# Optimization experiments

Hardware: AMD Instinct MI355X
Metric: run time of the kernel (lower is better)

The kernel has to match this reference:

```python
import jax, jax.numpy as jnp
import numpy as np

N_BATCH = 1024   # batch size (P=256 identities x K=4 instances)
M_PARTS = 8      # local stripes per image
D_FEAT = 128     # local feature dim
K_PER_ID = 4
MARGIN = 0.3
EPS = 1e-12


def setup_inputs() -> dict:
    key = jax.random.key(0)
    inputs = jax.random.normal(key, (N_BATCH, M_PARTS, D_FEAT), dtype=jnp.float32)
    labels = jnp.arange(N_BATCH, dtype=jnp.int64) // K_PER_ID  # equal samples per class
    return {"inputs": inputs, "labels": labels}


def _shortest_dist(dmat):
    """DTW-style monotone shortest path over the (m, n) grid.
    dmat: [m, n, N, N] -> returns [N, N].
    """
    m = dmat.shape[0]
    # first row: only moves to the right -> cumulative sum over j
    row = jnp.cumsum(dmat[0], axis=0)  # [n, N, N]
    inf = jnp.full(dmat.shape[2:], jnp.inf, dtype=dmat.dtype)

    def step(carry, inp):
        d_ij, up = inp                       # each [N, N]
        val = jnp.minimum(carry, up) + d_ij  # carry=inf at j=0 -> picks `up`
        return val, val

    for i in range(1, m):  # m is a small structural constant (stripes)
        _, row = jax.lax.scan(step, inf, (dmat[i], row))
    return row[-1]  # dist[m-1][n-1], shape [N, N]


def _local_dist(x):
    """x: [N, m, d] (already L2-normalized) -> pairwise aligned dist [N, N]."""
    N, m, d = x.shape
    xf = x.reshape(N * m, d)
    sq = jnp.sum(xf * xf, axis=1)
    dist = sq[:, None] + sq[None, :] - 2.0 * (xf @ xf.T)   # [Nm, Nm]
    dist = jnp.sqrt(jnp.clip(dist, EPS, None))
    dist = jnp.tanh(dist * 0.5)  # (e^d - 1) / (e^d + 1)
    dist = dist.reshape(N, m, N, m).transpose(1, 3, 0, 2)   # [m, n, N, N]
    return _shortest_dist(dist)


def reference(inputs, labels):
    # normalize local features to unit length
    x = inputs / (jnp.linalg.norm(inputs, axis=-1, keepdims=True) + EPS)
    dist_mat = _local_dist(x)  # [N, N]

    # hard example mining
    is_pos = labels[:, None] == labels[None, :]
    dist_ap = jnp.max(jnp.where(is_pos, dist_mat, -jnp.inf), axis=1)
    dist_an = jnp.min(jnp.where(is_pos, jnp.inf, dist_mat), axis=1)

    # MarginRankingLoss(margin)(dist_an, dist_ap, y=1)
    loss = jnp.mean(jnp.maximum(dist_ap - dist_an + MARGIN, 0.0))
    return loss
```

## Files before the change

### kernel.cpp

```cpp
#include <hip/hip_runtime.h>
#include <hip/hip_bf16.h>
#include <math.h>

#define NB 1024
#define MP 8
#define DF 128
#define NV (NB*MP)
#define EPSR 1e-12f
#define MARGIN_ 0.3f

#define GC0  0.4999965f
#define GC1 -0.0416276f
#define GC2  0.0040808f
#define GC3 -0.00035138f
#define GC4  0.00001765f

typedef __bf16 bf16x8 __attribute__((ext_vector_type(8)));
typedef float  f32x4  __attribute__((ext_vector_type(4)));

__global__ __launch_bounds__(256) void norm_kernel(const float* __restrict__ x,
                                                   unsigned short* __restrict__ xnb,
                                                   unsigned* __restrict__ ap_max,
                                                   unsigned* __restrict__ an_min) {
    if (blockIdx.x == 0) {
        for (int i = threadIdx.x; i < NB; i += 256) {
            ap_max[i] = 0u;
            an_min[i] = 0x7F800000u;
        }
    }
    const int wave = threadIdx.x >> 6;
    const int lane = threadIdx.x & 63;
    const int v = blockIdx.x * 4 + wave;
    const float e0 = x[v * DF + lane];
    const float e1 = x[v * DF + 64 + lane];
    float s = e0 * e0 + e1 * e1;
    #pragma unroll
    for (int off = 32; off > 0; off >>= 1) s += __shfl_xor(s, off);
    const float inv = 1.0f / (sqrtf(s) + EPSR);
    const __hip_bfloat16 b0 = __float2bfloat16(e0 * inv);
    const __hip_bfloat16 b1 = __float2bfloat16(e1 * inv);
    xnb[v * DF + lane]      = *(const unsigned short*)&b0;
    xnb[v * DF + 64 + lane] = *(const unsigned short*)&b1;
}

__global__ __launch_bounds__(256) void dist_kernel(const unsigned short* __restrict__ xnb,
                                                   const int* __restrict__ labels,
                                                   unsigned* __restrict__ ap_max,
                                                   unsigned* __restrict__ an_min) {
    __shared__ alignas(16) unsigned char smem[65536];
    unsigned short* As = (unsigned short*)smem;
    unsigned short* Bs = (unsigned short*)(smem + 32768);
    float* E = (float*)smem;

    const int idx = (int)blockIdx.x;
    float fsq = sqrtf(8.0f * (float)idx + 1.0f);
    int by = (int)((fsq - 1.0f) * 0.5f);
    while ((by + 1) * (by + 2) / 2 <= idx) ++by;
    while (by * (by + 1) / 2 > idx) --by;
    const int bx = idx - by * (by + 1) / 2;

    const int t    = threadIdx.x;
    const int wave = t >> 6;
    const int lane = t & 63;
    const int wr   = wave >> 1;
    const int wc   = wave & 1;
    const int aBase = bx * 16;
    const int bBase = by * 16;

    #pragma unroll
    for (int i = 0; i < 8; ++i) {
        const int ldi = t + i * 256;
        const int row = ldi >> 4;
        const int ch  = ldi & 15;
        const int p   = ch ^ (row & 15);
        const uint4 va = *(const uint4*)&xnb[(aBase * MP + row) * DF + ch * 8];
        const uint4 vb = *(const uint4*)&xnb[(bBase * MP + row) * DF + ch * 8];
        *(uint4*)&As[row * DF + p * 8] = va;
        *(uint4*)&Bs[row * DF + p * 8] = vb;
    }
    __syncthreads();

    f32x4 acc[4][4];
    #pragma unroll
    for (int tr = 0; tr < 4; ++tr)
        #pragma unroll
        for (int tc = 0; tc < 4; ++tc) acc[tr][tc] = (f32x4){0.f, 0.f, 0.f, 0.f};

    const int fr = lane & 15;
    const int fq = lane >> 4;
    #pragma unroll
    for (int ks = 0; ks < 4; ++ks) {
        bf16x8 af[4], bfr[4];
        const int ch = ks * 4 + fq;
        #pragma unroll
        for (int tr = 0; tr < 4; ++tr) {
            const int va = wr * 64 + tr * 16 + fr;
            af[tr] = *(const bf16x8*)&As[va * DF + (ch ^ fr) * 8];
        }
        #pragma unroll
        for (int tc = 0; tc < 4; ++tc) {
            const int vb = wc * 64 + tc * 16 + fr;
            bfr[tc] = *(const bf16x8*)&Bs[vb * DF + (ch ^ fr) * 8];
        }
        #pragma unroll
        for (int tr = 0; tr < 4; ++tr)
            #pragma unroll
            for (int tc = 0; tc < 4; ++tc)
                acc[tr][tc] = __builtin_amdgcn_mfma_f32_16x16x32_bf16(
                    af[tr], bfr[tc], acc[tr][tc], 0, 0, 0);
    }
    __syncthreads();

    #pragma unroll
    for (int tr = 0; tr < 4; ++tr) {
        const int r0 = wr * 64 + tr * 16 + fq * 4;
        const int aL = r0 >> 3;
        const int cqr = fq & 1;
        #pragma unroll
        for (int tc = 0; tc < 4; ++tc) {
            const int c  = wc * 64 + tc * 16 + fr;
            const int bL = c >> 3, j = c & 7;
            const int cq = (j << 1) | cqr;
            const int p  = (cq ^ bL) & 15;
            *(f32x4*)&E[(((aL << 4) + bL) << 6) + (p << 2)] = acc[tr][tc];
        }
    }
    __syncthreads();

    float g8[8][8];
    {
        const int bL = t & 15;
        #pragma unroll
        for (int cq = 0; cq < 16; ++cq) {
            const int p = (cq ^ bL) & 15;
            const f32x4 v = *(const f32x4*)&E[(t << 6) + (p << 2)];
            const int j = cq >> 1, ib = (cq & 1) * 4;
            #pragma unroll
            for (int g = 0; g < 4; ++g) {
                const float d2 = fmaxf(fmaf(-2.0f, v[g], 2.0f), EPSR);
                const float d  = __builtin_amdgcn_sqrtf(d2);
                const float pg = fmaf(fmaf(fmaf(fmaf(GC4, d2, GC3), d2, GC2),
                                           d2, GC1), d2, GC0);
                g8[ib + g][j] = d * pg;
            }
        }
    }

    float rowv[8];
    {
        float c = 0.0f;
        #pragma unroll
        for (int j = 0; j < 8; ++j) { c += g8[0][j]; rowv[j] = c; }
    }
    #pragma unroll
    for (int i = 1; i < 8; ++i) {
        float carry = INFINITY;
        #pragma unroll
        for (int j = 0; j < 8; ++j) {
            const float v = fminf(carry, rowv[j]) + g8[i][j];
            rowv[j] = v;
            carry = v;
        }
    }
    const float d = rowv[7];

    const int aG = aBase + (t >> 4);
    const int bG = bBase + (t & 15);
    const bool pos = (labels[aG] == labels[bG]);

    float an_v = pos ? INFINITY : d;
    float ap_v = pos ? d : 0.0f;
    #pragma unroll
    for (int off = 1; off <= 8; off <<= 1) {
        an_v = fminf(an_v, __shfl_xor(an_v, off));
        ap_v = fmaxf(ap_v, __shfl_xor(ap_v, off));
    }
    if ((t & 15) == 0) {
        atomicMin(&an_min[aG], __float_as_uint(an_v));
        if (ap_v > 0.0f) atomicMax(&ap_max[aG], __float_as_uint(ap_v));
    }

    if (bx != by) {
        float an_m = pos ? INFINITY : d;
        float ap_m = pos ? d : 0.0f;
        an_m = fminf(an_m, __shfl_xor(an_m, 16));
        an_m = fminf(an_m, __shfl_xor(an_m, 32));
        ap_m = fmaxf(ap_m, __shfl_xor(ap_m, 16));
        ap_m = fmaxf(ap_m, __shfl_xor(ap_m, 32));
        if (lane < 16) {
            const int bG2 = bBase + lane;
            atomicMin(&an_min[bG2], __float_as_uint(an_m));
            if (ap_m > 0.0f) atomicMax(&ap_max[bG2], __float_as_uint(ap_m));
        }
    }
}

__global__ __launch_bounds__(256) void loss_kernel(const unsigned* __restrict__ ap_max,
                                                   const unsigned* __restrict__ an_min,
                                                   float* __restrict__ out) {
    __shared__ float buf[4];
    const int wave = threadIdx.x >> 6;
    const int lane = threadIdx.x & 63;
    float s = 0.0f;
    for (int i = threadIdx.x; i < NB; i += 256) {
        const float ap = __uint_as_float(ap_max[i]);
        const float an = __uint_as_float(an_min[i]);
        s += fmaxf(ap - an + MARGIN_, 0.0f);
    }
    #pragma unroll
    for (int off = 32; off > 0; off >>= 1) s += __shfl_xor(s, off);
    if (lane == 0) buf[wave] = s;
    __syncthreads();
    if (threadIdx.x == 0) {
        out[0] = (buf[0] + buf[1] + buf[2] + buf[3]) * (1.0f / (float)NB);
    }
}

extern "C" void kernel_launch(void* const* d_in, const int* in_sizes, int n_in,
                              void* d_out, int out_size, void* d_ws, size_t ws_size,
                              hipStream_t stream) {
    const float* x      = (const float*)d_in[0];
    const int*   labels = (const int*)d_in[1];
    float* out = (float*)d_out;

    unsigned short* xnb = (unsigned short*)d_ws;
    unsigned* ap_max = (unsigned*)(xnb + (size_t)NV * DF);
    unsigned* an_min = ap_max + NB;

    const int ntiles = (NB / 16) * (NB / 16 + 1) / 2;

    norm_kernel<<<NV / 4, 256, 0, stream>>>(x, xnb, ap_max, an_min);
    dist_kernel<<<ntiles, 256, 0, stream>>>(xnb, labels, ap_max, an_min);
    loss_kernel<<<1, 256, 0, stream>>>(ap_max, an_min, out);
}
```

Baseline: 88.54 us.

## Halve LDS by K-chunked staging and fp16 transformed-distance exchange

The dist kernel now stages A and B tiles in two K-chunks of 64 through a 32KB LDS buffer instead of the full 128-wide tiles in 64KB. The sqrt/tanh transform is applied right after the MFMA in registers, and the results are stored to LDS as fp16 rather than fp32, which halves the exchange buffer. The aim is to allow more workgroups per CU by cutting LDS use. The costs are an extra barrier round, plus fp16 rounding of the per-stripe distances before the DTW path sum, which adds a small precision risk.

```diff
diff --git a/kernel.cpp b/kernel.cpp
--- a/kernel.cpp
+++ b/kernel.cpp
@@ -15,8 +15,10 @@
 #define GC3 -0.00035138f
 #define GC4  0.00001765f
 
-typedef __bf16 bf16x8 __attribute__((ext_vector_type(8)));
-typedef float  f32x4  __attribute__((ext_vector_type(4)));
+typedef __bf16    bf16x8 __attribute__((ext_vector_type(8)));
+typedef float     f32x4  __attribute__((ext_vector_type(4)));
+typedef _Float16  f16x4  __attribute__((ext_vector_type(4)));
+typedef _Float16  f16x8  __attribute__((ext_vector_type(8)));
 
 __global__ __launch_bounds__(256) void norm_kernel(const float* __restrict__ x,
                                                    unsigned short* __restrict__ xnb,
@@ -47,10 +49,10 @@
                                                    const int* __restrict__ labels,
                                                    unsigned* __restrict__ ap_max,
                                                    unsigned* __restrict__ an_min) {
-    __shared__ alignas(16) unsigned char smem[65536];
+    __shared__ alignas(16) unsigned char smem[32768];
     unsigned short* As = (unsigned short*)smem;
-    unsigned short* Bs = (unsigned short*)(smem + 32768);
-    float* E = (float*)smem;
+    unsigned short* Bs = (unsigned short*)(smem + 16384);
+    unsigned short* E  = (unsigned short*)smem;
 
     const int idx = (int)blockIdx.x;
     float fsq = sqrtf(8.0f * (float)idx + 1.0f);
@@ -67,97 +69,101 @@
     const int aBase = bx * 16;
     const int bBase = by * 16;
 
-    #pragma unroll
-    for (int i = 0; i < 8; ++i) {
-        const int ldi = t + i * 256;
-        const int row = ldi >> 4;
-        const int ch  = ldi & 15;
-        const int p   = ch ^ (row & 15);
-        const uint4 va = *(const uint4*)&xnb[(aBase * MP + row) * DF + ch * 8];
-        const uint4 vb = *(const uint4*)&xnb[(bBase * MP + row) * DF + ch * 8];
-        *(uint4*)&As[row * DF + p * 8] = va;
-        *(uint4*)&Bs[row * DF + p * 8] = vb;
-    }
-    __syncthreads();
-
-    f32x4 acc[4][4];
-    #pragma unroll
-    for (int tr = 0; tr < 4; ++tr)
-        #pragma unroll
-        for (int tc = 0; tc < 4; ++tc) acc[tr][tc] = (f32x4){0.f, 0.f, 0.f, 0.f};
-
     const int fr = lane & 15;
     const int fq = lane >> 4;
-    #pragma unroll
-    for (int ks = 0; ks < 4; ++ks) {
-        bf16x8 af[4], bfr[4];
-        const int ch = ks * 4 + fq;
-        #pragma unroll
-        for (int tr = 0; tr < 4; ++tr) {
-            const int va = wr * 64 + tr * 16 + fr;
-            af[tr] = *(const bf16x8*)&As[va * DF + (ch ^ fr) * 8];
-        }
-        #pragma unroll
-        for (int tc = 0; tc < 4; ++tc) {
-            const int vb = wc * 64 + tc * 16 + fr;
-            bfr[tc] = *(const bf16x8*)&Bs[vb * DF + (ch ^ fr) * 8];
-        }
-        #pragma unroll
-        for (int tr = 0; tr < 4; ++tr)
-            #pragma unroll
-            for (int tc = 0; tc < 4; ++tc)
-                acc[tr][tc] = __builtin_amdgcn_mfma_f32_16x16x32_bf16(
-                    af[tr], bfr[tc], acc[tr][tc], 0, 0, 0);
+
+    f32x4 acc[4][4];
+    #pragma unroll
+    for (int tr = 0; tr < 4; ++tr)
+        #pragma unroll
+        for (int tc = 0; tc < 4; ++tc) acc[tr][tc] = (f32x4){0.f, 0.f, 0.f, 0.f};
+
+    #pragma unroll
+    for (int kci = 0; kci < 2; ++kci) {
+        const int kc = kci * 64;
+        if (kci) __syncthreads();
+        #pragma unroll
+        for (int i = 0; i < 8; ++i) {
+            const int ldi  = t + i * 256;
+            const int side = ldi >> 10;
+            const int r    = (ldi >> 3) & 127;
+            const int ch   = ldi & 7;
+            const int gv   = (side ? bBase : aBase) * MP + r;
+            const uint4 v  = *(const uint4*)&xnb[gv * DF + kc + ch * 8];
+            unsigned short* dst = side ? Bs : As;
+            *(uint4*)&dst[r * 64 + ((ch ^ (r & 7)) * 8)] = v;
+        }
+        __syncthreads();
+
+        #pragma unroll
+        for (int ksl = 0; ksl < 2; ++ksl) {
+            bf16x8 af[4], bfr[4];
+            const int ch = ksl * 4 + fq;
+            #pragma unroll
+            for (int tr = 0; tr < 4; ++tr) {
+                const int va = wr * 64 + tr * 16 + fr;
+                af[tr] = *(const bf16x8*)&As[va * 64 + ((ch ^ (fr & 7)) * 8)];
+            }
+            #pragma unroll
+            for (int tc = 0; tc < 4; ++tc) {
+                const int vb = wc * 64 + tc * 16 + fr;
+                bfr[tc] = *(const bf16x8*)&Bs[vb * 64 + ((ch ^ (fr & 7)) * 8)];
+            }
+            #pragma unroll
+            for (int tr = 0; tr < 4; ++tr)
+                #pragma unroll
+                for (int tc = 0; tc < 4; ++tc)
+                    acc[tr][tc] = __builtin_amdgcn_mfma_f32_16x16x32_bf16(
+                        af[tr], bfr[tc], acc[tr][tc], 0, 0, 0);
+        }
     }
     __syncthreads();
 
     #pragma unroll
     for (int tr = 0; tr < 4; ++tr) {
-        const int r0 = wr * 64 + tr * 16 + fq * 4;
-        const int aL = r0 >> 3;
-        const int cqr = fq & 1;
+        const int r0   = wr * 64 + tr * 16 + fq * 4;
+        const int aL   = r0 >> 3;
+        const int half = fq & 1;
         #pragma unroll
         for (int tc = 0; tc < 4; ++tc) {
             const int c  = wc * 64 + tc * 16 + fr;
             const int bL = c >> 3, j = c & 7;
-            const int cq = (j << 1) | cqr;
-            const int p  = (cq ^ bL) & 15;
-            *(f32x4*)&E[(((aL << 4) + bL) << 6) + (p << 2)] = acc[tr][tc];
-        }
-    }
-    __syncthreads();
-
-    float g8[8][8];
-    {
-        const int bL = t & 15;
-        #pragma unroll
-        for (int cq = 0; cq < 16; ++cq) {
-            const int p = (cq ^ bL) & 15;
-            const f32x4 v = *(const f32x4*)&E[(t << 6) + (p << 2)];
-            const int j = cq >> 1, ib = (cq & 1) * 4;
+            f16x4 hv;
             #pragma unroll
             for (int g = 0; g < 4; ++g) {
-                const float d2 = fmaxf(fmaf(-2.0f, v[g], 2.0f), EPSR);
+                const float d2 = fmaxf(fmaf(-2.0f, acc[tr][tc][g], 2.0f), 0.0f);
                 const float d  = __builtin_amdgcn_sqrtf(d2);
                 const float pg = fmaf(fmaf(fmaf(fmaf(GC4, d2, GC3), d2, GC2),
                                            d2, GC1), d2, GC0);
-                g8[ib + g][j] = d * pg;
+                hv[g] = (_Float16)(d * pg);
             }
-        }
+            const int p   = (aL << 4) + bL;
+            const int pos = j ^ (bL & 7);
+            *(f16x4*)&E[(p << 6) + (pos << 3) + (half << 2)] = hv;
+        }
+    }
+    __syncthreads();
+
+    f16x8 colv[8];
+    {
+        const int s = t & 7;
+        #pragma unroll
+        for (int j = 0; j < 8; ++j)
+            colv[j] = *(const f16x8*)&E[(t << 6) + ((j ^ s) << 3)];
     }
 
     float rowv[8];
     {
         float c = 0.0f;
         #pragma unroll
-        for (int j = 0; j < 8; ++j) { c += g8[0][j]; rowv[j] = c; }
+        for (int j = 0; j < 8; ++j) { c += (float)colv[j][0]; rowv[j] = c; }
     }
     #pragma unroll
     for (int i = 1; i < 8; ++i) {
         float carry = INFINITY;
         #pragma unroll
         for (int j = 0; j < 8; ++j) {
-            const float v = fminf(carry, rowv[j]) + g8[i][j];
+            const float v = fminf(carry, rowv[j]) + (float)colv[j][i];
             rowv[j] = v;
             carry = v;
         }
```

Result: faster. 86.71 us (-2.1%).
